# Kernel tuning notes

Hardware: AMD Instinct MI355X
Metric: run time of the kernel (lower is better)

## Reference

```python
import jax, jax.numpy as jnp
import numpy as np


def _conv1d(x, w):
    # x: (B, W, Cin), w: (K, Cin, Cout), SAME padding, stride 1
    return jax.lax.conv_general_dilated(
        x, w, window_strides=(1,), padding='SAME',
        dimension_numbers=('NWC', 'WIO', 'NWC'))


def setup_inputs() -> dict:
    key = jax.random.key(0)
    ks = jax.random.split(key, 5)
    B, T, F, C, K = 64, 64, 256, 64, 9  # batch, num_frames, frame_size(noise_size), filters, kernel
    z = jax.random.normal(ks[0], (B, T, F, 1), dtype=jnp.float32)
    h0 = jax.random.normal(ks[1], (B, F, C), dtype=jnp.float32)
    c0 = jax.random.normal(ks[2], (B, F, C), dtype=jnp.float32)
    Wx = jax.random.normal(ks[3], (K, 1, 4 * C), dtype=jnp.float32) * 0.1
    Wh = jax.random.normal(ks[4], (K, C, 4 * C), dtype=jnp.float32) * 0.1
    b = jnp.zeros((4 * C,), dtype=jnp.float32)
    return {'z': z, 'h0': h0, 'c0': c0, 'Wx': Wx, 'Wh': Wh, 'b': b}


def reference(z, h0, c0, Wx, Wh, b):
    # z: (B, T, F, 1); h0/c0: (B, F, C)
    B = z.shape[0]
    FORGET_BIAS = 1.0  # tf ConvLSTMCell default

    def step(carry, z_t):
        h, c = carry
        gates = _conv1d(z_t, Wx) + _conv1d(h, Wh) + b  # (B, F, 4C)
        i, j, f, o = jnp.split(gates, 4, axis=-1)       # tf gate order: i, new_input, f, o
        c_new = c * jax.nn.sigmoid(f + FORGET_BIAS) + jax.nn.sigmoid(i) * jnp.tanh(j)
        h_new = jnp.tanh(c_new) * jax.nn.sigmoid(o)
        # post_rnn_callback: tanh(mean over channels)
        out = jnp.tanh(jnp.mean(h_new, axis=-1))        # (B, F)
        return (h_new, c_new), out

    z_t_first = jnp.transpose(z, (1, 0, 2, 3))          # (T, B, F, 1)
    (_, _), outs = jax.lax.scan(step, (h0, c0), z_t_first)  # outs: (T, B, F)
    # concat frames along frame axis -> (B, T*F)
    return jnp.transpose(outs, (1, 0, 2)).reshape(B, -1)
```

## Files before the change

### kernel.cpp

```cpp
#include <hip/hip_runtime.h>
#include <hip/hip_bf16.h>

#define BB 64
#define TT 64
#define FF 256
#define CC 64
#define GG 256
#define HP 264
#define GST 264

using frag_ab = __attribute__((ext_vector_type(8))) short;
using f32x4   = __attribute__((ext_vector_type(4))) float;

__device__ __forceinline__ float sigmoidf_(float x) {
    return 1.0f / (1.0f + __expf(-x));
}
__device__ __forceinline__ float tanhf_(float x) {
    const float e = __expf(2.0f * x);
    return 1.0f - 2.0f / (e + 1.0f);
}
__device__ __forceinline__ void split2(float v, short* hi, short* lo) {
    __hip_bfloat16 h = __float2bfloat16(v);
    __hip_bfloat16 l = __float2bfloat16(v - __bfloat162float(h));
    *hi = *reinterpret_cast<short*>(&h);
    *lo = *reinterpret_cast<short*>(&l);
}

__global__ __launch_bounds__(256) void prep_kernel(
    const float* __restrict__ Wh, const float* __restrict__ Wx,
    const float* __restrict__ h0,
    short* __restrict__ WhPh, short* __restrict__ WhPl,
    short* __restrict__ WxTh, short* __restrict__ WxTl,
    short* __restrict__ hAh, short* __restrict__ hAl,
    short* __restrict__ hBh, short* __restrict__ hBl)
{
    const int n = blockIdx.x * 256 + threadIdx.x;
    if (n < BB * HP * CC) {
        const int c = n & 63;
        const int r = (n >> 6) % HP;
        const int b = n / (HP * CC);
        if (r < 4 || r >= 260) {
            hAh[n] = 0; hAl[n] = 0; hBh[n] = 0; hBl[n] = 0;
        } else {
            split2(h0[(b * FF + (r - 4)) * CC + c], &hAh[n], &hAl[n]);
        }
    }
    if (n < 9 * GG * CC) {
        const int c32 = n & 31;
        const int g = (n >> 5) & 255;
        const int p = n >> 13;
        const int k = p >> 1;
        const int cin = (p & 1) * 32 + c32;
        split2(Wh[(k * CC + cin) * GG + g], &WhPh[n], &WhPl[n]);
    }
    if (n < GG * 32) {
        const int kz = n & 31;
        const int g = n >> 5;
        split2(kz < 9 ? Wx[kz * GG + g] : 0.0f, &WxTh[n], &WxTl[n]);
    }
}

__global__ __launch_bounds__(512, 2) void convlstm_step(
    const float* __restrict__ z,
    const short* __restrict__ hinh, const short* __restrict__ hinl,
    const float* __restrict__ c_in,
    const short* __restrict__ WhPh, const short* __restrict__ WhPl,
    const short* __restrict__ WxTh, const short* __restrict__ WxTl,
    const float* __restrict__ bias,
    short* __restrict__ houth, short* __restrict__ houtl,
    float* __restrict__ c_out,
    float* __restrict__ out, int t)
{
    __shared__ __align__(16) char hbyh[72 * 128];
    __shared__ __align__(16) char hbyl[72 * 128];
    __shared__ __align__(16) char zbyh[64 * 64];
    __shared__ __align__(16) char zbyl[64 * 64];
    __shared__ __align__(16) float gbuf[32 * GST];

    const int b = blockIdx.x;
    const int f0 = blockIdx.y * 64;
    const int tid = threadIdx.x;
    const int lane = tid & 63;
    const int w = tid >> 6;

    const int rA = lane & 15;
    const int sA = lane >> 4;
    const int gbase = w * 32;
    const int bln = rA * 32 + sA * 8;

    frag_ab cb[4];
    {
        const int o0 = gbase * 32 + bln;
        cb[0] = *reinterpret_cast<const frag_ab*>(WhPh + o0);
        cb[1] = *reinterpret_cast<const frag_ab*>(WhPh + o0 + 512);
        cb[2] = *reinterpret_cast<const frag_ab*>(WhPl + o0);
        cb[3] = *reinterpret_cast<const frag_ab*>(WhPl + o0 + 512);
    }
    const int flE = tid >> 4;
    const int ch0E = (tid & 15) * 4;
    const int cixE0 = (b * FF + f0 + flE) * CC + ch0E;
    const int cixE1 = cixE0 + 32 * CC;
    const float4 cold0 = *reinterpret_cast<const float4*>(&c_in[cixE0]);
    const float4 cold1 = *reinterpret_cast<const float4*>(&c_in[cixE1]);
    const float bv0 = bias[gbase + rA];
    const float bv1 = bias[gbase + 16 + rA];

    for (int idx = tid; idx < 72 * 8; idx += 512) {
        const int row = idx >> 3, slot = idx & 7;
        const int off = (b * HP + f0 + row) * CC + slot * 8;
        const frag_ab vh = *reinterpret_cast<const frag_ab*>(hinh + off);
        const frag_ab vl = *reinterpret_cast<const frag_ab*>(hinl + off);
        const int a = row * 128 + ((slot ^ (row & 7)) << 4);
        *reinterpret_cast<frag_ab*>(&hbyh[a]) = vh;
        *reinterpret_cast<frag_ab*>(&hbyl[a]) = vl;
    }
    if (tid < 256) {
        const int row = tid >> 2, slot = tid & 3;
        const float* zr = z + ((long)b * TT + t) * FF;
        short vh[8], vl[8];
        #pragma unroll
        for (int j = 0; j < 8; ++j) {
            const int kz = slot * 8 + j;
            const int f = f0 + row - 4 + kz;
            const float val = (kz < 9 && f >= 0 && f < FF) ? zr[f] : 0.0f;
            split2(val, &vh[j], &vl[j]);
        }
        const int a = row * 64 + ((slot ^ (row & 3)) << 4);
        *reinterpret_cast<frag_ab*>(&zbyh[a]) = *reinterpret_cast<frag_ab*>(vh);
        *reinterpret_cast<frag_ab*>(&zbyl[a]) = *reinterpret_cast<frag_ab*>(vl);
    }
    __syncthreads();

    f32x4 acc[4][2];
    #pragma unroll
    for (int Mt = 0; Mt < 4; ++Mt) {
        acc[Mt][0] = (f32x4){bv0, bv0, bv0, bv0};
        acc[Mt][1] = (f32x4){bv1, bv1, bv1, bv1};
    }

    frag_ab cah[4], cal[4];
    #pragma unroll
    for (int Mt = 0; Mt < 4; ++Mt) {
        const int r = Mt * 16 + rA;
        const int a = r * 128 + ((sA ^ (r & 7)) << 4);
        cah[Mt] = *reinterpret_cast<const frag_ab*>(&hbyh[a]);
        cal[Mt] = *reinterpret_cast<const frag_ab*>(&hbyl[a]);
    }

    #pragma unroll
    for (int p = 0; p < 19; ++p) {
        frag_ab nah[4], nal[4], nb[4];
        if (p < 17) {
            const int pn = p + 1;
            const int k = pn >> 1, kk = pn & 1;
            const int sl = kk * 4 + sA;
            #pragma unroll
            for (int Mt = 0; Mt < 4; ++Mt) {
                const int r = Mt * 16 + rA + k;
                const int a = r * 128 + ((sl ^ (r & 7)) << 4);
                nah[Mt] = *reinterpret_cast<const frag_ab*>(&hbyh[a]);
                nal[Mt] = *reinterpret_cast<const frag_ab*>(&hbyl[a]);
            }
            const int o0 = (pn * GG + gbase) * 32 + bln;
            nb[0] = *reinterpret_cast<const frag_ab*>(WhPh + o0);
            nb[1] = *reinterpret_cast<const frag_ab*>(WhPh + o0 + 512);
            nb[2] = *reinterpret_cast<const frag_ab*>(WhPl + o0);
            nb[3] = *reinterpret_cast<const frag_ab*>(WhPl + o0 + 512);
        } else if (p == 17) {
            #pragma unroll
            for (int Mt = 0; Mt < 4; ++Mt) {
                const int r = Mt * 16 + rA;
                const int a = r * 64 + ((sA ^ (r & 3)) << 4);
                nah[Mt] = *reinterpret_cast<const frag_ab*>(&zbyh[a]);
                nal[Mt] = *reinterpret_cast<const frag_ab*>(&zbyl[a]);
            }
            const int o0 = gbase * 32 + bln;
            nb[0] = *reinterpret_cast<const frag_ab*>(WxTh + o0);
            nb[1] = *reinterpret_cast<const frag_ab*>(WxTh + o0 + 512);
            nb[2] = *reinterpret_cast<const frag_ab*>(WxTl + o0);
            nb[3] = *reinterpret_cast<const frag_ab*>(WxTl + o0 + 512);
        }
        __builtin_amdgcn_s_setprio(1);
        #pragma unroll
        for (int Mt = 0; Mt < 4; ++Mt) {
            acc[Mt][0] = __builtin_amdgcn_mfma_f32_16x16x32_bf16(cah[Mt], cb[0], acc[Mt][0], 0, 0, 0);
            acc[Mt][1] = __builtin_amdgcn_mfma_f32_16x16x32_bf16(cah[Mt], cb[1], acc[Mt][1], 0, 0, 0);
        }
        #pragma unroll
        for (int Mt = 0; Mt < 4; ++Mt) {
            acc[Mt][0] = __builtin_amdgcn_mfma_f32_16x16x32_bf16(cah[Mt], cb[2], acc[Mt][0], 0, 0, 0);
            acc[Mt][1] = __builtin_amdgcn_mfma_f32_16x16x32_bf16(cah[Mt], cb[3], acc[Mt][1], 0, 0, 0);
        }
        #pragma unroll
        for (int Mt = 0; Mt < 4; ++Mt) {
            acc[Mt][0] = __builtin_amdgcn_mfma_f32_16x16x32_bf16(cal[Mt], cb[0], acc[Mt][0], 0, 0, 0);
            acc[Mt][1] = __builtin_amdgcn_mfma_f32_16x16x32_bf16(cal[Mt], cb[1], acc[Mt][1], 0, 0, 0);
        }
        __builtin_amdgcn_s_setprio(0);
        if (p < 18) {
            #pragma unroll
            for (int Mt = 0; Mt < 4; ++Mt) { cah[Mt] = nah[Mt]; cal[Mt] = nal[Mt]; }
            cb[0] = nb[0]; cb[1] = nb[1]; cb[2] = nb[2]; cb[3] = nb[3];
        }
    }

    #pragma unroll
    for (int pass = 0; pass < 2; ++pass) {
        if (pass) __syncthreads();
        #pragma unroll
        for (int Mh = 0; Mh < 2; ++Mh) {
            const int Mt = pass * 2 + Mh;
            #pragma unroll
            for (int gtI = 0; gtI < 2; ++gtI) {
                const int g = gbase + gtI * 16 + rA;
                float* gp = &gbuf[(Mh * 16 + sA * 4) * GST + g];
                gp[0]       = acc[Mt][gtI][0];
                gp[GST]     = acc[Mt][gtI][1];
                gp[2 * GST] = acc[Mt][gtI][2];
                gp[3 * GST] = acc[Mt][gtI][3];
            }
        }
        __syncthreads();

        const int f = f0 + pass * 32 + flE;
        const float* gr = &gbuf[flE * GST];
        const f32x4 gi = *reinterpret_cast<const f32x4*>(gr + ch0E);
        const f32x4 gj = *reinterpret_cast<const f32x4*>(gr + 64 + ch0E);
        const f32x4 gf = *reinterpret_cast<const f32x4*>(gr + 128 + ch0E);
        const f32x4 go = *reinterpret_cast<const f32x4*>(gr + 192 + ch0E);

        const float4 cold = pass ? cold1 : cold0;
        const float co_[4] = {cold.x, cold.y, cold.z, cold.w};

        float hsum = 0.0f;
        float cv[4];
        short hh[4], hl[4];
        #pragma unroll
        for (int j = 0; j < 4; ++j) {
            const float cnew = co_[j] * sigmoidf_(gf[j] + 1.0f) + sigmoidf_(gi[j]) * tanhf_(gj[j]);
            const float hnew = tanhf_(cnew) * sigmoidf_(go[j]);
            cv[j] = cnew;
            split2(hnew, &hh[j], &hl[j]);
            hsum += hnew;
        }
        const int cix = (b * FF + f) * CC + ch0E;
        *reinterpret_cast<float4*>(&c_out[cix]) = make_float4(cv[0], cv[1], cv[2], cv[3]);
        const int hix = (b * HP + 4 + f) * CC + ch0E;
        *reinterpret_cast<uint2*>(&houth[hix]) = *reinterpret_cast<uint2*>(hh);
        *reinterpret_cast<uint2*>(&houtl[hix]) = *reinterpret_cast<uint2*>(hl);

        hsum += __shfl_xor(hsum, 1);
        hsum += __shfl_xor(hsum, 2);
        hsum += __shfl_xor(hsum, 4);
        hsum += __shfl_xor(hsum, 8);
        if ((tid & 15) == 0)
            out[(long)b * (TT * FF) + t * FF + f] = tanhf_(hsum * (1.0f / 64.0f));
    }
}

extern "C" void kernel_launch(void* const* d_in, const int* in_sizes, int n_in,
                              void* d_out, int out_size, void* d_ws, size_t ws_size,
                              hipStream_t stream) {
    const float* z    = (const float*)d_in[0];
    const float* h0   = (const float*)d_in[1];
    const float* c0   = (const float*)d_in[2];
    const float* Wx   = (const float*)d_in[3];
    const float* Wh   = (const float*)d_in[4];
    const float* bias = (const float*)d_in[5];
    float* out = (float*)d_out;

    const int SEp = BB * HP * CC;
    const int SE  = BB * FF * CC;
    short* hAh = (short*)d_ws;
    short* hAl = hAh + SEp;
    short* hBh = hAl + SEp;
    short* hBl = hBh + SEp;
    float* cW  = (float*)(hBl + SEp);
    short* WhPh = (short*)(cW + SE);
    short* WhPl = WhPh + 9 * GG * CC;
    short* WxTh = WhPl + 9 * GG * CC;
    short* WxTl = WxTh + GG * 32;

    prep_kernel<<<(SEp + 255) / 256, 256, 0, stream>>>(Wh, Wx, h0, WhPh, WhPl,
                                                       WxTh, WxTl, hAh, hAl, hBh, hBl);

    dim3 grid(BB, FF / 64);
    for (int t = 0; t < TT; ++t) {
        const short* hih = (t & 1) ? hBh : hAh;
        const short* hil = (t & 1) ? hBl : hAl;
        short* hoh = (t & 1) ? hAh : hBh;
        short* hol = (t & 1) ? hAl : hBl;
        const float* cin = (t == 0) ? c0 : cW;
        convlstm_step<<<grid, 512, 0, stream>>>(z, hih, hil, cin,
                                                WhPh, WhPl, WxTh, WxTl, bias,
                                                hoh, hol, cW, out, t);
    }
}
```

Before: 1.029 ms.

## Fuse all timesteps into one persistent cooperative kernel with grid sync

Replaces the 64 per-timestep launches with a single cooperative kernel that loops over time and uses grid.sync between steps. The cell state stays in registers and each block's own hidden rows stay in double-buffered LDS, so each step only fetches the 8 halo rows from global memory. The intent is to remove per-launch overhead and most of the global h/c traffic. In exchange it relies on grid-wide barriers, and it uses a single global h buffer, so a neighbour can overwrite halo rows before they are read within the same step. The A-fragment LDS prefetch across iterations is also dropped.

Result: slower. 3.355 ms (+226.2%).

```diff
diff --git a/kernel.cpp b/kernel.cpp
--- a/kernel.cpp
+++ b/kernel.cpp
@@ -1,5 +1,8 @@
 #include <hip/hip_runtime.h>
 #include <hip/hip_bf16.h>
+#include <hip/hip_cooperative_groups.h>
+
+namespace cg = cooperative_groups;
 
 #define BB 64
 #define TT 64
@@ -31,8 +34,7 @@
     const float* __restrict__ h0,
     short* __restrict__ WhPh, short* __restrict__ WhPl,
     short* __restrict__ WxTh, short* __restrict__ WxTl,
-    short* __restrict__ hAh, short* __restrict__ hAl,
-    short* __restrict__ hBh, short* __restrict__ hBl)
+    short* __restrict__ hGh, short* __restrict__ hGl)
 {
     const int n = blockIdx.x * 256 + threadIdx.x;
     if (n < BB * HP * CC) {
@@ -40,9 +42,9 @@
         const int r = (n >> 6) % HP;
         const int b = n / (HP * CC);
         if (r < 4 || r >= 260) {
-            hAh[n] = 0; hAl[n] = 0; hBh[n] = 0; hBl[n] = 0;
+            hGh[n] = 0; hGl[n] = 0;
         } else {
-            split2(h0[(b * FF + (r - 4)) * CC + c], &hAh[n], &hAl[n]);
+            split2(h0[(b * FF + (r - 4)) * CC + c], &hGh[n], &hGl[n]);
         }
     }
     if (n < 9 * GG * CC) {
@@ -60,22 +62,22 @@
     }
 }
 
-__global__ __launch_bounds__(512, 2) void convlstm_step(
+__global__ __launch_bounds__(512, 2) void convlstm_all(
     const float* __restrict__ z,
-    const short* __restrict__ hinh, const short* __restrict__ hinl,
-    const float* __restrict__ c_in,
+    short* __restrict__ hGh, short* __restrict__ hGl,
+    const float* __restrict__ c0,
     const short* __restrict__ WhPh, const short* __restrict__ WhPl,
     const short* __restrict__ WxTh, const short* __restrict__ WxTl,
     const float* __restrict__ bias,
-    short* __restrict__ houth, short* __restrict__ houtl,
-    float* __restrict__ c_out,
-    float* __restrict__ out, int t)
+    float* __restrict__ out)
 {
-    __shared__ __align__(16) char hbyh[72 * 128];
-    __shared__ __align__(16) char hbyl[72 * 128];
-    __shared__ __align__(16) char zbyh[64 * 64];
-    __shared__ __align__(16) char zbyl[64 * 64];
+    __shared__ __align__(16) char hbh[2][72 * 128];
+    __shared__ __align__(16) char hbl[2][72 * 128];
+    __shared__ __align__(16) char zbh[64 * 64];
+    __shared__ __align__(16) char zbl[64 * 64];
     __shared__ __align__(16) float gbuf[32 * GST];
+
+    cg::grid_group grid = cg::this_grid();
 
     const int b = blockIdx.x;
     const int f0 = blockIdx.y * 64;
@@ -87,6 +89,25 @@
     const int sA = lane >> 4;
     const int gbase = w * 32;
     const int bln = rA * 32 + sA * 8;
+
+    const float bv0 = bias[gbase + rA];
+    const float bv1 = bias[gbase + 16 + rA];
+
+    const int flE = tid >> 4;
+    const int ch0E = (tid & 15) * 4;
+    const int cix0 = (b * FF + f0 + flE) * CC + ch0E;
+    float4 cv0 = *reinterpret_cast<const float4*>(&c0[cix0]);
+    float4 cv1 = *reinterpret_cast<const float4*>(&c0[cix0 + 32 * CC]);
+
+    for (int idx = tid; idx < 72 * 8; idx += 512) {
+        const int row = idx >> 3, slot = idx & 7;
+        const int off = (b * HP + f0 + row) * CC + slot * 8;
+        const frag_ab vh = *reinterpret_cast<const frag_ab*>(hGh + off);
+        const frag_ab vl = *reinterpret_cast<const frag_ab*>(hGl + off);
+        const int a = row * 128 + ((slot ^ (row & 7)) << 4);
+        *reinterpret_cast<frag_ab*>(&hbh[0][a]) = vh;
+        *reinterpret_cast<frag_ab*>(&hbl[0][a]) = vl;
+    }
 
     frag_ab cb[4];
     {
@@ -96,165 +117,174 @@
         cb[2] = *reinterpret_cast<const frag_ab*>(WhPl + o0);
         cb[3] = *reinterpret_cast<const frag_ab*>(WhPl + o0 + 512);
     }
-    const int flE = tid >> 4;
-    const int ch0E = (tid & 15) * 4;
-    const int cixE0 = (b * FF + f0 + flE) * CC + ch0E;
-    const int cixE1 = cixE0 + 32 * CC;
-    const float4 cold0 = *reinterpret_cast<const float4*>(&c_in[cixE0]);
-    const float4 cold1 = *reinterpret_cast<const float4*>(&c_in[cixE1]);
-    const float bv0 = bias[gbase + rA];
-    const float bv1 = bias[gbase + 16 + rA];
-
-    for (int idx = tid; idx < 72 * 8; idx += 512) {
-        const int row = idx >> 3, slot = idx & 7;
-        const int off = (b * HP + f0 + row) * CC + slot * 8;
-        const frag_ab vh = *reinterpret_cast<const frag_ab*>(hinh + off);
-        const frag_ab vl = *reinterpret_cast<const frag_ab*>(hinl + off);
-        const int a = row * 128 + ((slot ^ (row & 7)) << 4);
-        *reinterpret_cast<frag_ab*>(&hbyh[a]) = vh;
-        *reinterpret_cast<frag_ab*>(&hbyl[a]) = vl;
-    }
-    if (tid < 256) {
-        const int row = tid >> 2, slot = tid & 3;
-        const float* zr = z + ((long)b * TT + t) * FF;
-        short vh[8], vl[8];
-        #pragma unroll
-        for (int j = 0; j < 8; ++j) {
-            const int kz = slot * 8 + j;
-            const int f = f0 + row - 4 + kz;
-            const float val = (kz < 9 && f >= 0 && f < FF) ? zr[f] : 0.0f;
-            split2(val, &vh[j], &vl[j]);
-        }
-        const int a = row * 64 + ((slot ^ (row & 3)) << 4);
-        *reinterpret_cast<frag_ab*>(&zbyh[a]) = *reinterpret_cast<frag_ab*>(vh);
-        *reinterpret_cast<frag_ab*>(&zbyl[a]) = *reinterpret_cast<frag_ab*>(vl);
-    }
-    __syncthreads();
-
-    f32x4 acc[4][2];
-    #pragma unroll
-    for (int Mt = 0; Mt < 4; ++Mt) {
-        acc[Mt][0] = (f32x4){bv0, bv0, bv0, bv0};
-        acc[Mt][1] = (f32x4){bv1, bv1, bv1, bv1};
-    }
-
-    frag_ab cah[4], cal[4];
-    #pragma unroll
-    for (int Mt = 0; Mt < 4; ++Mt) {
-        const int r = Mt * 16 + rA;
-        const int a = r * 128 + ((sA ^ (r & 7)) << 4);
-        cah[Mt] = *reinterpret_cast<const frag_ab*>(&hbyh[a]);
-        cal[Mt] = *reinterpret_cast<const frag_ab*>(&hbyl[a]);
-    }
-
-    #pragma unroll
-    for (int p = 0; p < 19; ++p) {
-        frag_ab nah[4], nal[4], nb[4];
-        if (p < 17) {
-            const int pn = p + 1;
-            const int k = pn >> 1, kk = pn & 1;
-            const int sl = kk * 4 + sA;
-            #pragma unroll
-            for (int Mt = 0; Mt < 4; ++Mt) {
-                const int r = Mt * 16 + rA + k;
-                const int a = r * 128 + ((sl ^ (r & 7)) << 4);
-                nah[Mt] = *reinterpret_cast<const frag_ab*>(&hbyh[a]);
-                nal[Mt] = *reinterpret_cast<const frag_ab*>(&hbyl[a]);
-            }
-            const int o0 = (pn * GG + gbase) * 32 + bln;
-            nb[0] = *reinterpret_cast<const frag_ab*>(WhPh + o0);
-            nb[1] = *reinterpret_cast<const frag_ab*>(WhPh + o0 + 512);
-            nb[2] = *reinterpret_cast<const frag_ab*>(WhPl + o0);
-            nb[3] = *reinterpret_cast<const frag_ab*>(WhPl + o0 + 512);
-        } else if (p == 17) {
-            #pragma unroll
-            for (int Mt = 0; Mt < 4; ++Mt) {
-                const int r = Mt * 16 + rA;
-                const int a = r * 64 + ((sA ^ (r & 3)) << 4);
-                nah[Mt] = *reinterpret_cast<const frag_ab*>(&zbyh[a]);
-                nal[Mt] = *reinterpret_cast<const frag_ab*>(&zbyl[a]);
-            }
-            const int o0 = gbase * 32 + bln;
-            nb[0] = *reinterpret_cast<const frag_ab*>(WxTh + o0);
-            nb[1] = *reinterpret_cast<const frag_ab*>(WxTh + o0 + 512);
-            nb[2] = *reinterpret_cast<const frag_ab*>(WxTl + o0);
-            nb[3] = *reinterpret_cast<const frag_ab*>(WxTl + o0 + 512);
-        }
-        __builtin_amdgcn_s_setprio(1);
+
+    #pragma unroll 1
+    for (int t = 0; t < TT; ++t) {
+        char* Hh = hbh[t & 1];
+        char* Hl = hbl[t & 1];
+        char* Nh = hbh[(t + 1) & 1];
+        char* Nl = hbl[(t + 1) & 1];
+
+        if (tid < 256) {
+            const int row = tid >> 2, slot = tid & 3;
+            const float* zr = z + ((long)b * TT + t) * FF;
+            short vh[8], vl[8];
+            #pragma unroll
+            for (int j = 0; j < 8; ++j) {
+                const int kz = slot * 8 + j;
+                const int f = f0 + row - 4 + kz;
+                const float val = (kz < 9 && f >= 0 && f < FF) ? zr[f] : 0.0f;
+                split2(val, &vh[j], &vl[j]);
+            }
+            const int a = row * 64 + ((slot ^ (row & 3)) << 4);
+            *reinterpret_cast<frag_ab*>(&zbh[a]) = *reinterpret_cast<frag_ab*>(vh);
+            *reinterpret_cast<frag_ab*>(&zbl[a]) = *reinterpret_cast<frag_ab*>(vl);
+        }
+        if (t > 0 && tid < 128) {
+            const int which = tid >> 6;
+            const int rr = tid & 63;
+            int row = rr >> 3;
+            row = (row < 4) ? row : row + 64;
+            const int slot = rr & 7;
+            const int off = (b * HP + f0 + row) * CC + slot * 8;
+            const int a = row * 128 + ((slot ^ (row & 7)) << 4);
+            if (which == 0)
+                *reinterpret_cast<frag_ab*>(&Hh[a]) = *reinterpret_cast<const frag_ab*>(hGh + off);
+            else
+                *reinterpret_cast<frag_ab*>(&Hl[a]) = *reinterpret_cast<const frag_ab*>(hGl + off);
+        }
+        __syncthreads();
+
+        f32x4 acc[4][2];
         #pragma unroll
         for (int Mt = 0; Mt < 4; ++Mt) {
-            acc[Mt][0] = __builtin_amdgcn_mfma_f32_16x16x32_bf16(cah[Mt], cb[0], acc[Mt][0], 0, 0, 0);
-            acc[Mt][1] = __builtin_amdgcn_mfma_f32_16x16x32_bf16(cah[Mt], cb[1], acc[Mt][1], 0, 0, 0);
-        }
+            acc[Mt][0] = (f32x4){bv0, bv0, bv0, bv0};
+            acc[Mt][1] = (f32x4){bv1, bv1, bv1, bv1};
+        }
+
         #pragma unroll
-        for (int Mt = 0; Mt < 4; ++Mt) {
-            acc[Mt][0] = __builtin_amdgcn_mfma_f32_16x16x32_bf16(cah[Mt], cb[2], acc[Mt][0], 0, 0, 0);
-            acc[Mt][1] = __builtin_amdgcn_mfma_f32_16x16x32_bf16(cah[Mt], cb[3], acc[Mt][1], 0, 0, 0);
-        }
+        for (int p = 0; p < 19; ++p) {
+            frag_ab nb[4];
+            if (p < 17) {
+                const int o0 = ((p + 1) * GG + gbase) * 32 + bln;
+                nb[0] = *reinterpret_cast<const frag_ab*>(WhPh + o0);
+                nb[1] = *reinterpret_cast<const frag_ab*>(WhPh + o0 + 512);
+                nb[2] = *reinterpret_cast<const frag_ab*>(WhPl + o0);
+                nb[3] = *reinterpret_cast<const frag_ab*>(WhPl + o0 + 512);
+            } else if (p == 17) {
+                const int o0 = gbase * 32 + bln;
+                nb[0] = *reinterpret_cast<const frag_ab*>(WxTh + o0);
+                nb[1] = *reinterpret_cast<const frag_ab*>(WxTh + o0 + 512);
+                nb[2] = *reinterpret_cast<const frag_ab*>(WxTl + o0);
+                nb[3] = *reinterpret_cast<const frag_ab*>(WxTl + o0 + 512);
+            }
+            frag_ab ah[4], al[4];
+            if (p < 18) {
+                const int k = p >> 1, kk = p & 1;
+                const int sl = kk * 4 + sA;
+                #pragma unroll
+                for (int Mt = 0; Mt < 4; ++Mt) {
+                    const int r = Mt * 16 + rA + k;
+                    const int a = r * 128 + ((sl ^ (r & 7)) << 4);
+                    ah[Mt] = *reinterpret_cast<const frag_ab*>(&Hh[a]);
+                    al[Mt] = *reinterpret_cast<const frag_ab*>(&Hl[a]);
+                }
+            } else {
+                #pragma unroll
+                for (int Mt = 0; Mt < 4; ++Mt) {
+                    const int r = Mt * 16 + rA;
+                    const int a = r * 64 + ((sA ^ (r & 3)) << 4);
+                    ah[Mt] = *reinterpret_cast<const frag_ab*>(&zbh[a]);
+                    al[Mt] = *reinterpret_cast<const frag_ab*>(&zbl[a]);
+                }
+            }
+            __builtin_amdgcn_s_setprio(1);
+            #pragma unroll
+            for (int Mt = 0; Mt < 4; ++Mt) {
+                acc[Mt][0] = __builtin_amdgcn_mfma_f32_16x16x32_bf16(ah[Mt], cb[0], acc[Mt][0], 0, 0, 0);
+                acc[Mt][1] = __builtin_amdgcn_mfma_f32_16x16x32_bf16(ah[Mt], cb[1], acc[Mt][1], 0, 0, 0);
+            }
+            #pragma unroll
+            for (int Mt = 0; Mt < 4; ++Mt) {
+                acc[Mt][0] = __builtin_amdgcn_mfma_f32_16x16x32_bf16(ah[Mt], cb[2], acc[Mt][0], 0, 0, 0);
+                acc[Mt][1] = __builtin_amdgcn_mfma_f32_16x16x32_bf16(ah[Mt], cb[3], acc[Mt][1], 0, 0, 0);
+            }
+            #pragma unroll
+            for (int Mt = 0; Mt < 4; ++Mt) {
+                acc[Mt][0] = __builtin_amdgcn_mfma_f32_16x16x32_bf16(al[Mt], cb[0], acc[Mt][0], 0, 0, 0);
+                acc[Mt][1] = __builtin_amdgcn_mfma_f32_16x16x32_bf16(al[Mt], cb[1], acc[Mt][1], 0, 0, 0);
+            }
+            __builtin_amdgcn_s_setprio(0);
+            if (p < 18) { cb[0] = nb[0]; cb[1] = nb[1]; cb[2] = nb[2]; cb[3] = nb[3]; }
+        }
+
+        {
+            const int o0 = gbase * 32 + bln;
+            cb[0] = *reinterpret_cast<const frag_ab*>(WhPh + o0);
+            cb[1] = *reinterpret_cast<const frag_ab*>(WhPh + o0 + 512);
+            cb[2] = *reinterpret_cast<const frag_ab*>(WhPl + o0);
+            cb[3] = *reinterpret_cast<const frag_ab*>(WhPl + o0 + 512);
+        }
+
         #pragma unroll
-        for (int Mt = 0; Mt < 4; ++Mt) {
-            acc[Mt][0] = __builtin_amdgcn_mfma_f32_16x16x32_bf16(cal[Mt], cb[0], acc[Mt][0], 0, 0, 0);
-            acc[Mt][1] = __builtin_amdgcn_mfma_f32_16x16x32_bf16(cal[Mt], cb[1], acc[Mt][1], 0, 0, 0);
-        }
-        __builtin_amdgcn_s_setprio(0);
-        if (p < 18) {
-            #pragma unroll
-            for (int Mt = 0; Mt < 4; ++Mt) { cah[Mt] = nah[Mt]; cal[Mt] = nal[Mt]; }
-            cb[0] = nb[0]; cb[1] = nb[1]; cb[2] = nb[2]; cb[3] = nb[3];
-        }
-    }
-
-    #pragma unroll
-    for (int pass = 0; pass < 2; ++pass) {
-        if (pass) __syncthreads();
-        #pragma unroll
-        for (int Mh = 0; Mh < 2; ++Mh) {
-            const int Mt = pass * 2 + Mh;
-            #pragma unroll
-            for (int gtI = 0; gtI < 2; ++gtI) {
-                const int g = gbase + gtI * 16 + rA;
-                float* gp = &gbuf[(Mh * 16 + sA * 4) * GST + g];
-                gp[0]       = acc[Mt][gtI][0];
-                gp[GST]     = acc[Mt][gtI][1];
-                gp[2 * GST] = acc[Mt][gtI][2];
-                gp[3 * GST] = acc[Mt][gtI][3];
-            }
-        }
-        __syncthreads();
-
-        const int f = f0 + pass * 32 + flE;
-        const float* gr = &gbuf[flE * GST];
-        const f32x4 gi = *reinterpret_cast<const f32x4*>(gr + ch0E);
-        const f32x4 gj = *reinterpret_cast<const f32x4*>(gr + 64 + ch0E);
-        const f32x4 gf = *reinterpret_cast<const f32x4*>(gr + 128 + ch0E);
-        const f32x4 go = *reinterpret_cast<const f32x4*>(gr + 192 + ch0E);
-
-        const float4 cold = pass ? cold1 : cold0;
-        const float co_[4] = {cold.x, cold.y, cold.z, cold.w};
-
-        float hsum = 0.0f;
-        float cv[4];
-        short hh[4], hl[4];
-        #pragma unroll
-        for (int j = 0; j < 4; ++j) {
-            const float cnew = co_[j] * sigmoidf_(gf[j] + 1.0f) + sigmoidf_(gi[j]) * tanhf_(gj[j]);
-            const float hnew = tanhf_(cnew) * sigmoidf_(go[j]);
-            cv[j] = cnew;
-            split2(hnew, &hh[j], &hl[j]);
-            hsum += hnew;
-        }
-        const int cix = (b * FF + f) * CC + ch0E;
-        *reinterpret_cast<float4*>(&c_out[cix]) = make_float4(cv[0], cv[1], cv[2], cv[3]);
-        const int hix = (b * HP + 4 + f) * CC + ch0E;
-        *reinterpret_cast<uint2*>(&houth[hix]) = *reinterpret_cast<uint2*>(hh);
-        *reinterpret_cast<uint2*>(&houtl[hix]) = *reinterpret_cast<uint2*>(hl);
-
-        hsum += __shfl_xor(hsum, 1);
-        hsum += __shfl_xor(hsum, 2);
-        hsum += __shfl_xor(hsum, 4);
-        hsum += __shfl_xor(hsum, 8);
-        if ((tid & 15) == 0)
-            out[(long)b * (TT * FF) + t * FF + f] = tanhf_(hsum * (1.0f / 64.0f));
+        for (int pass = 0; pass < 2; ++pass) {
+            if (pass) __syncthreads();
+            #pragma unroll
+            for (int Mh = 0; Mh < 2; ++Mh) {
+                const int Mt = pass * 2 + Mh;
+                #pragma unroll
+                for (int gtI = 0; gtI < 2; ++gtI) {
+                    const int g = gbase + gtI * 16 + rA;
+                    float* gp = &gbuf[(Mh * 16 + sA * 4) * GST + g];
+                    gp[0]       = acc[Mt][gtI][0];
+                    gp[GST]     = acc[Mt][gtI][1];
+                    gp[2 * GST] = acc[Mt][gtI][2];
+                    gp[3 * GST] = acc[Mt][gtI][3];
+                }
+            }
+            __syncthreads();
+
+            const int f = f0 + pass * 32 + flE;
+            const float* gr = &gbuf[flE * GST];
+            const f32x4 gi = *reinterpret_cast<const f32x4*>(gr + ch0E);
+            const f32x4 gj = *reinterpret_cast<const f32x4*>(gr + 64 + ch0E);
+            const f32x4 gf = *reinterpret_cast<const f32x4*>(gr + 128 + ch0E);
+            const f32x4 go = *reinterpret_cast<const f32x4*>(gr + 192 + ch0E);
+
+            float4& cvr = pass ? cv1 : cv0;
+            const float co_[4] = {cvr.x, cvr.y, cvr.z, cvr.w};
+
+            float hsum = 0.0f;
+            float cv[4];
+            short hh[4], hl[4];
+            #pragma unroll
+            for (int j = 0; j < 4; ++j) {
+                const float cnew = co_[j] * sigmoidf_(gf[j] + 1.0f) + sigmoidf_(gi[j]) * tanhf_(gj[j]);
+                const float hnew = tanhf_(cnew) * sigmoidf_(go[j]);
+                cv[j] = cnew;
+                split2(hnew, &hh[j], &hl[j]);
+                hsum += hnew;
+            }
+            cvr = make_float4(cv[0], cv[1], cv[2], cv[3]);
+
+            const int hix = (b * HP + 4 + f) * CC + ch0E;
+            *reinterpret_cast<uint2*>(&hGh[hix]) = *reinterpret_cast<uint2*>(hh);
+            *reinterpret_cast<uint2*>(&hGl[hix]) = *reinterpret_cast<uint2*>(hl);
+            const int r = pass * 32 + flE + 4;
+            const int slot = ch0E >> 3;
+            const int a = r * 128 + ((slot ^ (r & 7)) << 4) + (ch0E & 7) * 2;
+            *reinterpret_cast<uint2*>(&Nh[a]) = *reinterpret_cast<uint2*>(hh);
+            *reinterpret_cast<uint2*>(&Nl[a]) = *reinterpret_cast<uint2*>(hl);
+
+            hsum += __shfl_xor(hsum, 1);
+            hsum += __shfl_xor(hsum, 2);
+            hsum += __shfl_xor(hsum, 4);
+            hsum += __shfl_xor(hsum, 8);
+            if ((tid & 15) == 0)
+                out[(long)b * (TT * FF) + t * FF + f] = tanhf_(hsum * (1.0f / 64.0f));
+        }
+
+        if (t != TT - 1) grid.sync();
     }
 }
 
@@ -270,29 +300,22 @@
     float* out = (float*)d_out;
 
     const int SEp = BB * HP * CC;
-    const int SE  = BB * FF * CC;
-    short* hAh = (short*)d_ws;
-    short* hAl = hAh + SEp;
-    short* hBh = hAl + SEp;
-    short* hBl = hBh + SEp;
-    float* cW  = (float*)(hBl + SEp);
-    short* WhPh = (short*)(cW + SE);
+    short* hGh = (short*)d_ws;
+    short* hGl = hGh + SEp;
+    short* WhPh = hGl + SEp;
     short* WhPl = WhPh + 9 * GG * CC;
     short* WxTh = WhPl + 9 * GG * CC;
     short* WxTl = WxTh + GG * 32;
 
     prep_kernel<<<(SEp + 255) / 256, 256, 0, stream>>>(Wh, Wx, h0, WhPh, WhPl,
-                                                       WxTh, WxTl, hAh, hAl, hBh, hBl);
-
-    dim3 grid(BB, FF / 64);
-    for (int t = 0; t < TT; ++t) {
-        const short* hih = (t & 1) ? hBh : hAh;
-        const short* hil = (t & 1) ? hBl : hAl;
-        short* hoh = (t & 1) ? hAh : hBh;
-        short* hol = (t & 1) ? hAl : hBl;
-        const float* cin = (t == 0) ? c0 : cW;
-        convlstm_step<<<grid, 512, 0, stream>>>(z, hih, hil, cin,
-                                                WhPh, WhPl, WxTh, WxTl, bias,
-                                                hoh, hol, cW, out, t);
-    }
-}
+                                                       WxTh, WxTl, hGh, hGl);
+
+    void* args[] = {
+        (void*)&z, (void*)&hGh, (void*)&hGl, (void*)&c0,
+        (void*)&WhPh, (void*)&WhPl, (void*)&WxTh, (void*)&WxTl,
+        (void*)&bias, (void*)&out
+    };
+    hipLaunchCooperativeKernel((void*)convlstm_all,
+                               dim3(BB, FF / 64), dim3(512),
+                               args, 0, stream);
+}
```

## Switch gate GEMM to 32x32x16 MFMA with K=16 weight layout and reduced z padding

Applied to the files above, without the earlier changes.

Replaces the 16x16x32 bf16 MFMA tiling (4 M-tiles x 2 N-tiles per wave) with 32x32x16 MFMAs (2 M-tiles x 1 N-tile of 32 gates), repacking Wh/Wx weights into 16-wide K chunks and shrinking the z input padding from 32 to 16 taps. The aim is fewer MFMA instructions for the same bf16x3 split-precision work, plus less wasted K on the Wx term. Weight fragments are now prefetched two steps ahead from global memory. In exchange, A fragments are loaded from LDS within the same iteration instead of one step ahead, so LDS latency may be less hidden, and the loop runs 37 iterations instead of 19.

Measured after the change: 1.083 ms. 1.05x slower.

```diff
diff --git a/kernel.cpp b/kernel.cpp
--- a/kernel.cpp
+++ b/kernel.cpp
@@ -11,6 +11,7 @@
 
 using frag_ab = __attribute__((ext_vector_type(8))) short;
 using f32x4   = __attribute__((ext_vector_type(4))) float;
+using f32x16  = __attribute__((ext_vector_type(16))) float;
 
 __device__ __forceinline__ float sigmoidf_(float x) {
     return 1.0f / (1.0f + __expf(-x));
@@ -29,8 +30,8 @@
 __global__ __launch_bounds__(256) void prep_kernel(
     const float* __restrict__ Wh, const float* __restrict__ Wx,
     const float* __restrict__ h0,
-    short* __restrict__ WhPh, short* __restrict__ WhPl,
-    short* __restrict__ WxTh, short* __restrict__ WxTl,
+    short* __restrict__ WhBh, short* __restrict__ WhBl,
+    short* __restrict__ WxBh, short* __restrict__ WxBl,
     short* __restrict__ hAh, short* __restrict__ hAl,
     short* __restrict__ hBh, short* __restrict__ hBl)
 {
@@ -45,18 +46,18 @@
             split2(h0[(b * FF + (r - 4)) * CC + c], &hAh[n], &hAl[n]);
         }
     }
-    if (n < 9 * GG * CC) {
-        const int c32 = n & 31;
-        const int g = (n >> 5) & 255;
-        const int p = n >> 13;
-        const int k = p >> 1;
-        const int cin = (p & 1) * 32 + c32;
-        split2(Wh[(k * CC + cin) * GG + g], &WhPh[n], &WhPl[n]);
-    }
-    if (n < GG * 32) {
-        const int kz = n & 31;
-        const int g = n >> 5;
-        split2(kz < 9 ? Wx[kz * GG + g] : 0.0f, &WxTh[n], &WxTl[n]);
+    if (n < 36 * GG * 16) {
+        const int e = n & 15;
+        const int g = (n >> 4) & 255;
+        const int p = n >> 12;
+        const int k = p >> 2;
+        const int cin = (p & 3) * 16 + e;
+        split2(Wh[(k * CC + cin) * GG + g], &WhBh[n], &WhBl[n]);
+    }
+    if (n < GG * 16) {
+        const int e = n & 15;
+        const int g = n >> 4;
+        split2(e < 9 ? Wx[e * GG + g] : 0.0f, &WxBh[n], &WxBl[n]);
     }
 }
 
@@ -64,8 +65,8 @@
     const float* __restrict__ z,
     const short* __restrict__ hinh, const short* __restrict__ hinl,
     const float* __restrict__ c_in,
-    const short* __restrict__ WhPh, const short* __restrict__ WhPl,
-    const short* __restrict__ WxTh, const short* __restrict__ WxTl,
+    const short* __restrict__ WhBh, const short* __restrict__ WhBl,
+    const short* __restrict__ WxBh, const short* __restrict__ WxBl,
     const float* __restrict__ bias,
     short* __restrict__ houth, short* __restrict__ houtl,
     float* __restrict__ c_out,
@@ -73,8 +74,8 @@
 {
     __shared__ __align__(16) char hbyh[72 * 128];
     __shared__ __align__(16) char hbyl[72 * 128];
-    __shared__ __align__(16) char zbyh[64 * 64];
-    __shared__ __align__(16) char zbyl[64 * 64];
+    __shared__ __align__(16) char zbh[64 * 48];
+    __shared__ __align__(16) char zbl[64 * 48];
     __shared__ __align__(16) float gbuf[32 * GST];
 
     const int b = blockIdx.x;
@@ -83,27 +84,26 @@
     const int lane = tid & 63;
     const int w = tid >> 6;
 
-    const int rA = lane & 15;
-    const int sA = lane >> 4;
+    const int l31 = lane & 31;
+    const int hf = lane >> 5;
     const int gbase = w * 32;
-    const int bln = rA * 32 + sA * 8;
-
-    frag_ab cb[4];
+    const int gq = gbase + l31;
+
+    frag_ab b0h, b0l, b1h, b1l;
     {
-        const int o0 = gbase * 32 + bln;
-        cb[0] = *reinterpret_cast<const frag_ab*>(WhPh + o0);
-        cb[1] = *reinterpret_cast<const frag_ab*>(WhPh + o0 + 512);
-        cb[2] = *reinterpret_cast<const frag_ab*>(WhPl + o0);
-        cb[3] = *reinterpret_cast<const frag_ab*>(WhPl + o0 + 512);
-    }
+        const int o0 = gq * 16 + hf * 8;
+        const int o1 = (256 + gq) * 16 + hf * 8;
+        b0h = *reinterpret_cast<const frag_ab*>(WhBh + o0);
+        b0l = *reinterpret_cast<const frag_ab*>(WhBl + o0);
+        b1h = *reinterpret_cast<const frag_ab*>(WhBh + o1);
+        b1l = *reinterpret_cast<const frag_ab*>(WhBl + o1);
+    }
+    const float bv = bias[gq];
     const int flE = tid >> 4;
     const int ch0E = (tid & 15) * 4;
     const int cixE0 = (b * FF + f0 + flE) * CC + ch0E;
-    const int cixE1 = cixE0 + 32 * CC;
     const float4 cold0 = *reinterpret_cast<const float4*>(&c_in[cixE0]);
-    const float4 cold1 = *reinterpret_cast<const float4*>(&c_in[cixE1]);
-    const float bv0 = bias[gbase + rA];
-    const float bv1 = bias[gbase + 16 + rA];
+    const float4 cold1 = *reinterpret_cast<const float4*>(&c_in[cixE0 + 32 * CC]);
 
     for (int idx = tid; idx < 72 * 8; idx += 512) {
         const int row = idx >> 3, slot = idx & 7;
@@ -114,111 +114,79 @@
         *reinterpret_cast<frag_ab*>(&hbyh[a]) = vh;
         *reinterpret_cast<frag_ab*>(&hbyl[a]) = vl;
     }
-    if (tid < 256) {
-        const int row = tid >> 2, slot = tid & 3;
+    if (tid < 128) {
+        const int row = tid >> 1, half = tid & 1;
         const float* zr = z + ((long)b * TT + t) * FF;
         short vh[8], vl[8];
         #pragma unroll
         for (int j = 0; j < 8; ++j) {
-            const int kz = slot * 8 + j;
+            const int kz = half * 8 + j;
             const int f = f0 + row - 4 + kz;
             const float val = (kz < 9 && f >= 0 && f < FF) ? zr[f] : 0.0f;
             split2(val, &vh[j], &vl[j]);
         }
-        const int a = row * 64 + ((slot ^ (row & 3)) << 4);
-        *reinterpret_cast<frag_ab*>(&zbyh[a]) = *reinterpret_cast<frag_ab*>(vh);
-        *reinterpret_cast<frag_ab*>(&zbyl[a]) = *reinterpret_cast<frag_ab*>(vl);
+        const int a = row * 48 + half * 16;
+        *reinterpret_cast<frag_ab*>(&zbh[a]) = *reinterpret_cast<frag_ab*>(vh);
+        *reinterpret_cast<frag_ab*>(&zbl[a]) = *reinterpret_cast<frag_ab*>(vl);
     }
     __syncthreads();
 
-    f32x4 acc[4][2];
+    f32x16 acc[2];
     #pragma unroll
-    for (int Mt = 0; Mt < 4; ++Mt) {
-        acc[Mt][0] = (f32x4){bv0, bv0, bv0, bv0};
-        acc[Mt][1] = (f32x4){bv1, bv1, bv1, bv1};
-    }
-
-    frag_ab cah[4], cal[4];
+    for (int r = 0; r < 16; ++r) { acc[0][r] = bv; acc[1][r] = bv; }
+
     #pragma unroll
-    for (int Mt = 0; Mt < 4; ++Mt) {
-        const int r = Mt * 16 + rA;
-        const int a = r * 128 + ((sA ^ (r & 7)) << 4);
-        cah[Mt] = *reinterpret_cast<const frag_ab*>(&hbyh[a]);
-        cal[Mt] = *reinterpret_cast<const frag_ab*>(&hbyl[a]);
-    }
-
-    #pragma unroll
-    for (int p = 0; p < 19; ++p) {
-        frag_ab nah[4], nal[4], nb[4];
-        if (p < 17) {
-            const int pn = p + 1;
-            const int k = pn >> 1, kk = pn & 1;
-            const int sl = kk * 4 + sA;
+    for (int p = 0; p < 37; ++p) {
+        frag_ab nbh, nbl;
+        if (p + 2 < 36) {
+            const int o = ((p + 2) * 256 + gq) * 16 + hf * 8;
+            nbh = *reinterpret_cast<const frag_ab*>(WhBh + o);
+            nbl = *reinterpret_cast<const frag_ab*>(WhBl + o);
+        } else if (p + 2 == 36) {
+            const int o = gq * 16 + hf * 8;
+            nbh = *reinterpret_cast<const frag_ab*>(WxBh + o);
+            nbl = *reinterpret_cast<const frag_ab*>(WxBl + o);
+        }
+        frag_ab ah[2], al[2];
+        if (p < 36) {
+            const int k = p >> 2, s = p & 3;
+            const int sl = s * 2 + hf;
             #pragma unroll
-            for (int Mt = 0; Mt < 4; ++Mt) {
-                const int r = Mt * 16 + rA + k;
+            for (int Mt = 0; Mt < 2; ++Mt) {
+                const int r = Mt * 32 + l31 + k;
                 const int a = r * 128 + ((sl ^ (r & 7)) << 4);
-                nah[Mt] = *reinterpret_cast<const frag_ab*>(&hbyh[a]);
-                nal[Mt] = *reinterpret_cast<const frag_ab*>(&hbyl[a]);
+                ah[Mt] = *reinterpret_cast<const frag_ab*>(&hbyh[a]);
+                al[Mt] = *reinterpret_cast<const frag_ab*>(&hbyl[a]);
             }
-            const int o0 = (pn * GG + gbase) * 32 + bln;
-            nb[0] = *reinterpret_cast<const frag_ab*>(WhPh + o0);
-            nb[1] = *reinterpret_cast<const frag_ab*>(WhPh + o0 + 512);
-            nb[2] = *reinterpret_cast<const frag_ab*>(WhPl + o0);
-            nb[3] = *reinterpret_cast<const frag_ab*>(WhPl + o0 + 512);
-        } else if (p == 17) {
+        } else {
             #pragma unroll
-            for (int Mt = 0; Mt < 4; ++Mt) {
-                const int r = Mt * 16 + rA;
-                const int a = r * 64 + ((sA ^ (r & 3)) << 4);
-                nah[Mt] = *reinterpret_cast<const frag_ab*>(&zbyh[a]);
-                nal[Mt] = *reinterpret_cast<const frag_ab*>(&zbyl[a]);
+            for (int Mt = 0; Mt < 2; ++Mt) {
+                const int a = (Mt * 32 + l31) * 48 + hf * 16;
+                ah[Mt] = *reinterpret_cast<const frag_ab*>(&zbh[a]);
+                al[Mt] = *reinterpret_cast<const frag_ab*>(&zbl[a]);
             }
-            const int o0 = gbase * 32 + bln;
-            nb[0] = *reinterpret_cast<const frag_ab*>(WxTh + o0);
-            nb[1] = *reinterpret_cast<const frag_ab*>(WxTh + o0 + 512);
-            nb[2] = *reinterpret_cast<const frag_ab*>(WxTl + o0);
-            nb[3] = *reinterpret_cast<const frag_ab*>(WxTl + o0 + 512);
         }
         __builtin_amdgcn_s_setprio(1);
         #pragma unroll
-        for (int Mt = 0; Mt < 4; ++Mt) {
-            acc[Mt][0] = __builtin_amdgcn_mfma_f32_16x16x32_bf16(cah[Mt], cb[0], acc[Mt][0], 0, 0, 0);
-            acc[Mt][1] = __builtin_amdgcn_mfma_f32_16x16x32_bf16(cah[Mt], cb[1], acc[Mt][1], 0, 0, 0);
-        }
-        #pragma unroll
-        for (int Mt = 0; Mt < 4; ++Mt) {
-            acc[Mt][0] = __builtin_amdgcn_mfma_f32_16x16x32_bf16(cah[Mt], cb[2], acc[Mt][0], 0, 0, 0);
-            acc[Mt][1] = __builtin_amdgcn_mfma_f32_16x16x32_bf16(cah[Mt], cb[3], acc[Mt][1], 0, 0, 0);
-        }
-        #pragma unroll
-        for (int Mt = 0; Mt < 4; ++Mt) {
-            acc[Mt][0] = __builtin_amdgcn_mfma_f32_16x16x32_bf16(cal[Mt], cb[0], acc[Mt][0], 0, 0, 0);
-            acc[Mt][1] = __builtin_amdgcn_mfma_f32_16x16x32_bf16(cal[Mt], cb[1], acc[Mt][1], 0, 0, 0);
-        }
+        for (int Mt = 0; Mt < 2; ++Mt)
+            acc[Mt] = __builtin_amdgcn_mfma_f32_32x32x16_bf16(ah[Mt], b0h, acc[Mt], 0, 0, 0);
+        #pragma unroll
+        for (int Mt = 0; Mt < 2; ++Mt)
+            acc[Mt] = __builtin_amdgcn_mfma_f32_32x32x16_bf16(ah[Mt], b0l, acc[Mt], 0, 0, 0);
+        #pragma unroll
+        for (int Mt = 0; Mt < 2; ++Mt)
+            acc[Mt] = __builtin_amdgcn_mfma_f32_32x32x16_bf16(al[Mt], b0h, acc[Mt], 0, 0, 0);
         __builtin_amdgcn_s_setprio(0);
-        if (p < 18) {
-            #pragma unroll
-            for (int Mt = 0; Mt < 4; ++Mt) { cah[Mt] = nah[Mt]; cal[Mt] = nal[Mt]; }
-            cb[0] = nb[0]; cb[1] = nb[1]; cb[2] = nb[2]; cb[3] = nb[3];
-        }
+        b0h = b1h; b0l = b1l; b1h = nbh; b1l = nbl;
     }
 
     #pragma unroll
     for (int pass = 0; pass < 2; ++pass) {
         if (pass) __syncthreads();
         #pragma unroll
-        for (int Mh = 0; Mh < 2; ++Mh) {
-            const int Mt = pass * 2 + Mh;
-            #pragma unroll
-            for (int gtI = 0; gtI < 2; ++gtI) {
-                const int g = gbase + gtI * 16 + rA;
-                float* gp = &gbuf[(Mh * 16 + sA * 4) * GST + g];
-                gp[0]       = acc[Mt][gtI][0];
-                gp[GST]     = acc[Mt][gtI][1];
-                gp[2 * GST] = acc[Mt][gtI][2];
-                gp[3 * GST] = acc[Mt][gtI][3];
-            }
+        for (int reg = 0; reg < 16; ++reg) {
+            const int crow = (reg & 3) + 8 * (reg >> 2) + 4 * hf;
+            gbuf[crow * GST + gq] = acc[pass][reg];
         }
         __syncthreads();
 
@@ -276,13 +244,13 @@
     short* hBh = hAl + SEp;
     short* hBl = hBh + SEp;
     float* cW  = (float*)(hBl + SEp);
-    short* WhPh = (short*)(cW + SE);
-    short* WhPl = WhPh + 9 * GG * CC;
-    short* WxTh = WhPl + 9 * GG * CC;
-    short* WxTl = WxTh + GG * 32;
-
-    prep_kernel<<<(SEp + 255) / 256, 256, 0, stream>>>(Wh, Wx, h0, WhPh, WhPl,
-                                                       WxTh, WxTl, hAh, hAl, hBh, hBl);
+    short* WhBh = (short*)(cW + SE);
+    short* WhBl = WhBh + 36 * GG * 16;
+    short* WxBh = WhBl + 36 * GG * 16;
+    short* WxBl = WxBh + GG * 16;
+
+    prep_kernel<<<(SEp + 255) / 256, 256, 0, stream>>>(Wh, Wx, h0, WhBh, WhBl,
+                                                       WxBh, WxBl, hAh, hAl, hBh, hBl);
 
     dim3 grid(BB, FF / 64);
     for (int t = 0; t < TT; ++t) {
@@ -292,7 +260,7 @@
         short* hol = (t & 1) ? hAl : hBl;
         const float* cin = (t == 0) ? c0 : cW;
         convlstm_step<<<grid, 512, 0, stream>>>(z, hih, hil, cin,
-                                                WhPh, WhPl, WxTh, WxTl, bias,
+                                                WhBh, WhBl, WxBh, WxBl, bias,
                                                 hoh, hol, cW, out, t);
     }
 }
```
